# Kernel optimization log

Hardware: AMD Instinct MI355X
Metric: run time of the kernel (lower is better)

The kernel has to match this reference:

```python
import jax, jax.numpy as jnp
import numpy as np

NEG = -1000000.0  # mask fill value used by original sequence_mask

def setup_inputs() -> dict:
    key = jax.random.key(0)
    k1, k2, k3, k4 = jax.random.split(key, 4)
    B, S, D = 32, 2048, 64
    queries = jax.random.normal(k1, (B, S, D), dtype=jnp.float32)
    keys = jax.random.normal(k2, (B, S, D), dtype=jnp.float32)
    values = jax.random.normal(k3, (B, S, D), dtype=jnp.float32)
    valid_lens = jax.random.randint(k4, (B,), 1, S + 1, dtype=jnp.int64)
    return {"queries": queries, "keys": keys, "values": values, "valid_lens": valid_lens}

def reference(queries, keys, values, valid_lens):
    d = queries.shape[-1]
    # [B, Sq, Sk]
    scores = jnp.einsum('bqd,bkd->bqk', queries, keys) / jnp.sqrt(jnp.asarray(d, queries.dtype))
    # valid_lens is 1D: one length per batch row, broadcast over all query rows
    kv_idx = jnp.arange(scores.shape[-1])  # [Sk]
    mask = kv_idx[None, None, :] < valid_lens[:, None, None]  # [B,1,Sk] broadcast
    scores = jnp.where(mask, scores, jnp.asarray(NEG, scores.dtype))
    weights = jax.nn.softmax(scores, axis=-1)
    # dropout p=0.0 -> identity
    return jnp.einsum('bqk,bkd->bqd', weights, values)
```

## Files before the change

### kernel.cpp

```cpp
#include <hip/hip_runtime.h>
#include <hip/hip_bf16.h>

typedef __attribute__((ext_vector_type(8))) short bf16x8;
typedef __attribute__((ext_vector_type(4))) float f32x4;
typedef __attribute__((ext_vector_type(16))) float f32x16;

#define BATCH 32
#define SEQ   2048
#define PSTR  20
#define KSTR  72
#define VSTR  36
#define LOG2E 1.44269504088896340736f
#define QSCALE (0.125f * LOG2E)
#define NEGL  (-1000000.0f * LOG2E)

__device__ __forceinline__ unsigned int pk2(float lo, float hi) {
    __hip_bfloat162 h2 = __float22bfloat162_rn(make_float2(lo, hi));
    return *reinterpret_cast<unsigned int*>(&h2);
}

__device__ __forceinline__ void dma16(const short* g, short* l) {
    __builtin_amdgcn_global_load_lds((const __attribute__((address_space(1))) void*)g,
                                     (__attribute__((address_space(3))) void*)l, 16, 0, 0);
}

__device__ __forceinline__ void plswap(unsigned int& a, unsigned int& b) {
    asm volatile("v_permlane32_swap_b32 %0, %1" : "+v"(a), "+v"(b));
}

__global__ void prep_vl(const int* __restrict__ VL, int* __restrict__ meta) {
    __shared__ int sv[BATCH];
    const int t = threadIdx.x;
    int odd = (t < 16) ? VL[2 * t + 1] : 0;
    const bool is64 = (__ballot(odd != 0) == 0ULL);
    if (t < BATCH) {
        int x = is64 ? VL[2 * t] : VL[t];
        x = x < 0 ? 0 : (x > SEQ ? SEQ : x);
        sv[t] = x;
    }
    __syncthreads();
    if (t < BATCH) {
        const int x = sv[t];
        int rank = 0;
        for (int j = 0; j < BATCH; ++j) {
            const int y = sv[j];
            rank += (y > x) || (y == x && j < t);
        }
        meta[rank] = x;
        meta[BATCH + rank] = t;
    }
}

__global__ __launch_bounds__(256) void prepkv(const float* __restrict__ Kp,
                                              const float* __restrict__ Vp,
                                              const int* __restrict__ VL,
                                              short* __restrict__ Kb,
                                              short* __restrict__ Vt,
                                              int* __restrict__ meta) {
    __shared__ unsigned int l[64 * VSTR];
    __shared__ int sv[BATCH];
    __shared__ int svl;
    const int tid = threadIdx.x;
    if (blockIdx.x == BATCH * 32) {
        if (tid < 64) {
            int odd = (tid < 16) ? VL[2 * tid + 1] : 0;
            const bool is64 = (__ballot(odd != 0) == 0ULL);
            if (tid < BATCH) {
                int x = is64 ? VL[2 * tid] : VL[tid];
                x = x < 0 ? 0 : (x > SEQ ? SEQ : x);
                sv[tid] = x;
            }
            asm volatile("s_waitcnt lgkmcnt(0)" ::: "memory");
            if (tid < BATCH) {
                const int x = sv[tid];
                int rank = 0;
                for (int j = 0; j < BATCH; ++j) {
                    const int y = sv[j];
                    rank += (y > x) || (y == x && j < tid);
                }
                meta[rank] = x;
                meta[BATCH + rank] = tid;
            }
        }
        return;
    }
    const int b = blockIdx.x >> 5, kt = blockIdx.x & 31, kb = kt * 64;
    if (tid < 64) {
        int odd = (tid < 16) ? VL[2 * tid + 1] : 0;
        const bool is64 = (__ballot(odd != 0) == 0ULL);
        if (tid == 0) {
            int x = is64 ? VL[2 * b] : VL[b];
            x = x < 0 ? 0 : (x > SEQ ? SEQ : x);
            svl = x;
        }
    }
    __syncthreads();
    if (kb >= svl) return;
    const float* Kv = Kp + ((size_t)b * SEQ + kb) * 64;
    const float* Vb = Vp + ((size_t)b * SEQ + kb) * 64;
    #pragma unroll
    for (int h = 0; h < 4; ++h) {
        const int c = tid + h * 256;
        const int row = c >> 4, col = (c & 15) * 4;
        f32x4 x = *(const f32x4*)(Kv + row * 64 + col);
        unsigned int* dst = (unsigned int*)(Kb + ((size_t)b * SEQ + kb + row) * 64 + col);
        dst[0] = pk2(x[0], x[1]); dst[1] = pk2(x[2], x[3]);
    }
    #pragma unroll
    for (int h = 0; h < 2; ++h) {
        const int u = tid + h * 256;
        const int d4 = (u & 3) + ((u >> 7) << 2);
        const int kp = (u >> 2) & 31;
        f32x4 a = *(const f32x4*)(Vb + (2 * kp) * 64 + d4 * 4);
        f32x4 c = *(const f32x4*)(Vb + (2 * kp + 1) * 64 + d4 * 4);
        #pragma unroll
        for (int j = 0; j < 4; ++j)
            l[(d4 * 4 + j) * VSTR + kp] = pk2(a[j], c[j]);
    }
    __syncthreads();
    const int d = tid >> 2, cg = tid & 3;
    unsigned int w[8];
    #pragma unroll
    for (int j = 0; j < 8; ++j) w[j] = l[d * VSTR + cg * 8 + j];
    unsigned int* dst = (unsigned int*)Vt + ((size_t)(b * 32 + kt) * 64 + d) * 32 + cg * 8;
    #pragma unroll
    for (int j = 0; j < 8; ++j) dst[j] = w[j];
}

__global__ __launch_bounds__(256, 4)
void attn_fwd(const float* __restrict__ Qp, const short* __restrict__ Kb,
              const short* __restrict__ Vt, const int* __restrict__ meta,
              float* __restrict__ Out) {
    constexpr int S = SEQ;
    __shared__ short bK2[2 * 4096];
    __shared__ short bV3[3 * 4096];

    const int tid  = threadIdx.x;
    const int wave = tid >> 6, lane = tid & 63;
    const int r31 = lane & 31, hi = lane >> 5;
    const int l7  = lane & 7;
    const int qh = wave >> 1, kh = wave & 1;

    const int g  = blockIdx.x >> 8;
    const int k8 = (blockIdx.x >> 5) & 7;
    const int qt = blockIdx.x & 31;
    const int slot = (g << 3) + ((g & 1) ? 7 - k8 : k8);

    const int vl = meta[slot], batch = meta[BATCH + slot];
    const int ntiles = (vl + 63) >> 6;

    const short* Kbb = Kb + (size_t)batch * S * 64;
    const short* Vtb = Vt + (size_t)batch * 32 * 4096;

    const int r8 = lane >> 3, s8 = lane & 7, csw = s8 ^ r8;
    const short* gK0 = Kbb + (wave * 16 + r8) * 64 + csw * 8;
    const short* gV0 = Vtb + (wave * 16 + r8) * 64 + csw * 8;
    short* lK0 = &bK2[wave * 16 * 64];
    short* lV0 = &bV3[wave * 16 * 64];

    bf16x8 qf[4];
    {
        const float* qb = Qp + ((size_t)batch * S + qt * 64 + qh * 32 + r31) * 64 + hi * 8;
        #pragma unroll
        for (int kf = 0; kf < 4; ++kf) {
            f32x4 a = *(const f32x4*)(qb + kf * 16);
            f32x4 c = *(const f32x4*)(qb + kf * 16 + 4);
            union { bf16x8 v; unsigned int u[4]; } qq;
            qq.u[0] = pk2(a[0] * QSCALE, a[1] * QSCALE);
            qq.u[1] = pk2(a[2] * QSCALE, a[3] * QSCALE);
            qq.u[2] = pk2(c[0] * QSCALE, c[1] * QSCALE);
            qq.u[3] = pk2(c[2] * QSCALE, c[3] * QSCALE);
            qf[kf] = qq.v;
        }
    }

    f32x16 o0, o1, zv;
    #pragma unroll
    for (int r = 0; r < 16; ++r) { o0[r] = 0.f; o1[r] = 0.f; zv[r] = 0.f; }
    float lpart = 0.f;
    const int krow = kh * 32 + r31;

    int vP = 16384, vC = 0, vN = 8192;
    union { bf16x8 v; unsigned int u[4]; } pf0, pf1;

    if (ntiles > 0) {
        dma16(gK0,       lK0);
        dma16(gK0 + 512, lK0 + 512);
        dma16(gV0,       lV0);
        dma16(gV0 + 512, lV0 + 512);
    }

    for (int kt = 0; kt < ntiles; ++kt) {
        __syncthreads();
        if (kt + 1 < ntiles) {
            const int ko = (kt + 1) * 4096;
            short* ktgt = lK0 + (((kt + 1) & 1) << 12);
            short* vtgt = (short*)((char*)lV0 + vN);
            dma16(gK0 + ko,       ktgt);
            dma16(gK0 + ko + 512, ktgt + 512);
            dma16(gV0 + ko,       vtgt);
            dma16(gV0 + ko + 512, vtgt + 512);
        }

        const char* cK = (const char*)bK2 + ((kt & 1) << 13);
        f32x16 st;
        __builtin_amdgcn_s_setprio(1);
        {
            bf16x8 k0 = *(const bf16x8*)(cK + krow * 128 + (((0 + hi) ^ l7) << 4));
            bf16x8 k1 = *(const bf16x8*)(cK + krow * 128 + (((2 + hi) ^ l7) << 4));
            bf16x8 k2 = *(const bf16x8*)(cK + krow * 128 + (((4 + hi) ^ l7) << 4));
            bf16x8 k3 = *(const bf16x8*)(cK + krow * 128 + (((6 + hi) ^ l7) << 4));
            st = __builtin_amdgcn_mfma_f32_32x32x16_bf16(k0, qf[0], zv, 0, 0, 0);
            st = __builtin_amdgcn_mfma_f32_32x32x16_bf16(k1, qf[1], st, 0, 0, 0);
            st = __builtin_amdgcn_mfma_f32_32x32x16_bf16(k2, qf[2], st, 0, 0, 0);
            st = __builtin_amdgcn_mfma_f32_32x32x16_bf16(k3, qf[3], st, 0, 0, 0);
        }
        if (kt > 0) {
            const char* cV = (const char*)bV3 + vP;
            bf16x8 vf0 = *(const bf16x8*)(cV + r31 * 128 + (((kh * 4 + hi) ^ l7) << 4));
            o0 = __builtin_amdgcn_mfma_f32_32x32x16_bf16(vf0, pf0.v, o0, 0, 0, 0);
            bf16x8 vf1 = *(const bf16x8*)(cV + r31 * 128 + (((kh * 4 + 2 + hi) ^ l7) << 4));
            o0 = __builtin_amdgcn_mfma_f32_32x32x16_bf16(vf1, pf1.v, o0, 0, 0, 0);
            bf16x8 vf2 = *(const bf16x8*)(cV + (32 + r31) * 128 + (((kh * 4 + hi) ^ l7) << 4));
            o1 = __builtin_amdgcn_mfma_f32_32x32x16_bf16(vf2, pf0.v, o1, 0, 0, 0);
            bf16x8 vf3 = *(const bf16x8*)(cV + (32 + r31) * 128 + (((kh * 4 + 2 + hi) ^ l7) << 4));
            o1 = __builtin_amdgcn_mfma_f32_32x32x16_bf16(vf3, pf1.v, o1, 0, 0, 0);
        }
        __builtin_amdgcn_s_setprio(0);

        const int rem = vl - (kt * 64 + kh * 32);
        if (rem < 32) {
            #pragma unroll
            for (int r = 0; r < 16; ++r) {
                const int kl = 4 * hi + (r & 3) + 8 * (r >> 2);
                st[r] = (kl < rem) ? st[r] : NEGL;
            }
        }

        #pragma unroll
        for (int r = 0; r < 16; ++r) st[r] = exp2f(st[r]);
        {
            const float a0 = (st[0] + st[1]) + (st[2] + st[3]);
            const float a1 = (st[4] + st[5]) + (st[6] + st[7]);
            const float a2 = (st[8] + st[9]) + (st[10] + st[11]);
            const float a3 = (st[12] + st[13]) + (st[14] + st[15]);
            lpart += (a0 + a1) + (a2 + a3);
        }

        {
            unsigned int x0 = pk2(st[0], st[1]),   y0 = pk2(st[4], st[5]);
            unsigned int x1 = pk2(st[2], st[3]),   y1 = pk2(st[6], st[7]);
            plswap(x0, y0); plswap(x1, y1);
            pf0.u[0] = x0; pf0.u[1] = x1; pf0.u[2] = y0; pf0.u[3] = y1;
            unsigned int x2 = pk2(st[8], st[9]),   y2 = pk2(st[12], st[13]);
            unsigned int x3 = pk2(st[10], st[11]), y3 = pk2(st[14], st[15]);
            plswap(x2, y2); plswap(x3, y3);
            pf1.u[0] = x2; pf1.u[1] = x3; pf1.u[2] = y2; pf1.u[3] = y3;
        }

        const int t_ = vP; vP = vC; vC = vN; vN = t_;
    }

    {
        const char* cV = (const char*)bV3 + vP;
        __builtin_amdgcn_s_setprio(1);
        bf16x8 vf0 = *(const bf16x8*)(cV + r31 * 128 + (((kh * 4 + hi) ^ l7) << 4));
        o0 = __builtin_amdgcn_mfma_f32_32x32x16_bf16(vf0, pf0.v, o0, 0, 0, 0);
        bf16x8 vf1 = *(const bf16x8*)(cV + r31 * 128 + (((kh * 4 + 2 + hi) ^ l7) << 4));
        o0 = __builtin_amdgcn_mfma_f32_32x32x16_bf16(vf1, pf1.v, o0, 0, 0, 0);
        bf16x8 vf2 = *(const bf16x8*)(cV + (32 + r31) * 128 + (((kh * 4 + hi) ^ l7) << 4));
        o1 = __builtin_amdgcn_mfma_f32_32x32x16_bf16(vf2, pf0.v, o1, 0, 0, 0);
        bf16x8 vf3 = *(const bf16x8*)(cV + (32 + r31) * 128 + (((kh * 4 + 2 + hi) ^ l7) << 4));
        o1 = __builtin_amdgcn_mfma_f32_32x32x16_bf16(vf3, pf1.v, o1, 0, 0, 0);
        __builtin_amdgcn_s_setprio(0);
    }

    float lw = lpart + __shfl_xor(lpart, 32);

    __syncthreads();
    float* mrg = (float*)bK2;
    float* lm  = (float*)bV3;
    if (kh == 1) {
        #pragma unroll
        for (int r = 0; r < 16; ++r) mrg[qh * 2048 + r * 64 + lane] = o0[r];
        #pragma unroll
        for (int r = 0; r < 16; ++r) mrg[qh * 2048 + (16 + r) * 64 + lane] = o1[r];
        lm[qh * 64 + lane] = lw;
    }
    __syncthreads();
    if (kh == 0) {
        #pragma unroll
        for (int r = 0; r < 16; ++r) o0[r] += mrg[qh * 2048 + r * 64 + lane];
        #pragma unroll
        for (int r = 0; r < 16; ++r) o1[r] += mrg[qh * 2048 + (16 + r) * 64 + lane];
        lw += lm[qh * 64 + lane];
        const float inv = (lw > 0.f) ? 1.0f / lw : 0.f;
        const size_t orow = ((size_t)batch * S + qt * 64 + qh * 32 + r31) * 64;
        #pragma unroll
        for (int g4 = 0; g4 < 4; ++g4) {
            f32x4 w;
            #pragma unroll
            for (int j = 0; j < 4; ++j) w[j] = o0[g4 * 4 + j] * inv;
            *(f32x4*)(Out + orow + g4 * 8 + hi * 4) = w;
        }
        #pragma unroll
        for (int g4 = 0; g4 < 4; ++g4) {
            f32x4 w;
            #pragma unroll
            for (int j = 0; j < 4; ++j) w[j] = o1[g4 * 4 + j] * inv;
            *(f32x4*)(Out + orow + 32 + g4 * 8 + hi * 4) = w;
        }
    }
}

__device__ __forceinline__ void load_tile_fb(const float* __restrict__ Kb,
                                             const float* __restrict__ Vb,
                                             int tid, f32x4 kv[4], f32x4 vv[4]) {
    #pragma unroll
    for (int h = 0; h < 4; ++h) {
        const int c = tid + h * 256;
        kv[h] = *(const f32x4*)(Kb + (c >> 4) * 64 + (c & 15) * 4);
    }
    #pragma unroll
    for (int h = 0; h < 2; ++h) {
        const int u  = tid + h * 256;
        const int d4 = (u & 3) + ((u >> 7) << 2);
        const int kp = (u >> 2) & 31;
        vv[2 * h]     = *(const f32x4*)(Vb + (2 * kp) * 64 + d4 * 4);
        vv[2 * h + 1] = *(const f32x4*)(Vb + (2 * kp + 1) * 64 + d4 * 4);
    }
}

__global__ __launch_bounds__(256, 4)
void attn_fb(const float* __restrict__ Qp, const float* __restrict__ Kp,
             const float* __restrict__ Vp, const int* __restrict__ meta,
             float* __restrict__ Out) {
    constexpr int S = SEQ;
    constexpr int qtiles = S >> 6;
    __shared__ short        lK [64 * KSTR];
    __shared__ unsigned int lVt[64 * VSTR];
    __shared__ unsigned int lPt[4 * 32 * PSTR];
    const int tid = threadIdx.x;
    const int wave = tid >> 6, lane = tid & 63;
    const int l15 = lane & 15, grp = lane >> 4;
    const int slot = blockIdx.x / qtiles, qt = blockIdx.x % qtiles;
    const int vl = meta[slot], batch = meta[BATCH + slot];
    const int ntiles = (vl + 63) >> 6;
    const float* Kb = Kp + (size_t)batch * S * 64;
    const float* Vb = Vp + (size_t)batch * S * 64;
    bf16x8 qf[2];
    {
        const float* qb = Qp + ((size_t)batch * S + qt * 64 + wave * 16 + l15) * 64 + grp * 8;
        #pragma unroll
        for (int kf = 0; kf < 2; ++kf) {
            f32x4 a = *(const f32x4*)(qb + kf * 32);
            f32x4 b = *(const f32x4*)(qb + kf * 32 + 4);
            union { bf16x8 v; unsigned int u[4]; } qq;
            qq.u[0] = pk2(a[0], a[1]); qq.u[1] = pk2(a[2], a[3]);
            qq.u[2] = pk2(b[0], b[1]); qq.u[3] = pk2(b[2], b[3]);
            qf[kf] = qq.v;
        }
    }
    f32x4 o[4] = {{0.f,0.f,0.f,0.f},{0.f,0.f,0.f,0.f},{0.f,0.f,0.f,0.f},{0.f,0.f,0.f,0.f}};
    float mrun = -INFINITY, lrun = 0.f;
    unsigned int* pw = &lPt[wave * 32 * PSTR];
    f32x4 kv[4], vv[4];
    if (ntiles > 0) load_tile_fb(Kb, Vb, tid, kv, vv);
    for (int kt = 0; kt < ntiles; ++kt) {
        const int kb = kt * 64;
        __syncthreads();
        #pragma unroll
        for (int h = 0; h < 4; ++h) {
            const int c = tid + h * 256;
            const int row = c >> 4, col = (c & 15) * 4;
            union { f32x4 f; float e[4]; } x; x.f = kv[h];
            unsigned int* dst = (unsigned int*)&lK[row * KSTR + col];
            dst[0] = pk2(x.e[0], x.e[1]); dst[1] = pk2(x.e[2], x.e[3]);
        }
        #pragma unroll
        for (int h = 0; h < 2; ++h) {
            const int u  = tid + h * 256;
            const int d4 = (u & 3) + ((u >> 7) << 2);
            const int kp = (u >> 2) & 31;
            union { f32x4 f; float e[4]; } a, b;
            a.f = vv[2 * h]; b.f = vv[2 * h + 1];
            #pragma unroll
            for (int j = 0; j < 4; ++j)
                lVt[(d4 * 4 + j) * VSTR + kp] = pk2(a.e[j], b.e[j]);
        }
        if (kt + 1 < ntiles) load_tile_fb(Kb + (size_t)(kb + 64) * 64, Vb + (size_t)(kb + 64) * 64, tid, kv, vv);
        __syncthreads();
        f32x4 st[4] = {{0.f,0.f,0.f,0.f},{0.f,0.f,0.f,0.f},{0.f,0.f,0.f,0.f},{0.f,0.f,0.f,0.f}};
        #pragma unroll
        for (int kf = 0; kf < 2; ++kf) {
            #pragma unroll
            for (int ct = 0; ct < 4; ++ct) {
                bf16x8 kfr = *(const bf16x8*)&lK[(ct * 16 + l15) * KSTR + kf * 32 + grp * 8];
                st[ct] = __builtin_amdgcn_mfma_f32_16x16x32_bf16(kfr, qf[kf], st[ct], 0, 0, 0);
            }
        }
        #pragma unroll
        for (int ct = 0; ct < 4; ++ct)
            #pragma unroll
            for (int r = 0; r < 4; ++r) {
                const bool valid = (kb + ct * 16 + grp * 4 + r) < vl;
                st[ct][r] = valid ? st[ct][r] * (0.125f * LOG2E) : NEGL;
            }
        float t0 = fmaxf(fmaxf(st[0][0], st[0][1]), fmaxf(st[0][2], st[0][3]));
        float t1 = fmaxf(fmaxf(st[1][0], st[1][1]), fmaxf(st[1][2], st[1][3]));
        float t2 = fmaxf(fmaxf(st[2][0], st[2][1]), fmaxf(st[2][2], st[2][3]));
        float t3 = fmaxf(fmaxf(st[3][0], st[3][1]), fmaxf(st[3][2], st[3][3]));
        float tm = fmaxf(fmaxf(t0, t1), fmaxf(t2, t3));
        tm = fmaxf(tm, __shfl_xor(tm, 16));
        tm = fmaxf(tm, __shfl_xor(tm, 32));
        const float mnew  = fmaxf(mrun, tm);
        const float alpha = exp2f(mrun - mnew);
        mrun = mnew;
        lrun *= alpha;
        #pragma unroll
        for (int dt = 0; dt < 4; ++dt)
            #pragma unroll
            for (int r = 0; r < 4; ++r) o[dt][r] *= alpha;
        float rs = 0.f;
        #pragma unroll
        for (int ct = 0; ct < 4; ++ct) {
            #pragma unroll
            for (int r = 0; r < 4; ++r) {
                st[ct][r] = exp2f(st[ct][r] - mrun);
                rs += st[ct][r];
            }
            #pragma unroll
            for (int a = 0; a < 2; ++a)
                pw[(ct * 8 + grp * 2 + a) * PSTR + l15] = pk2(st[ct][2 * a], st[ct][2 * a + 1]);
        }
        rs += __shfl_xor(rs, 16);
        rs += __shfl_xor(rs, 32);
        lrun += rs;
        asm volatile("s_waitcnt lgkmcnt(0)" ::: "memory");
        #pragma unroll
        for (int kk = 0; kk < 2; ++kk) {
            union { bf16x8 v; unsigned int u[4]; } pf;
            #pragma unroll
            for (int jj = 0; jj < 4; ++jj)
                pf.u[jj] = pw[(kk * 16 + grp * 4 + jj) * PSTR + l15];
            #pragma unroll
            for (int dt = 0; dt < 4; ++dt) {
                bf16x8 vf = *(const bf16x8*)&lVt[(dt * 16 + l15) * VSTR + kk * 16 + grp * 4];
                o[dt] = __builtin_amdgcn_mfma_f32_16x16x32_bf16(vf, pf.v, o[dt], 0, 0, 0);
            }
        }
    }
    const float inv = (lrun > 0.f) ? 1.0f / lrun : 0.f;
    const size_t orow = ((size_t)batch * S + qt * 64 + wave * 16 + l15) * 64;
    #pragma unroll
    for (int dt = 0; dt < 4; ++dt) {
        f32x4 w = o[dt];
        w[0] *= inv; w[1] *= inv; w[2] *= inv; w[3] *= inv;
        *(f32x4*)(Out + orow + dt * 16 + grp * 4) = w;
    }
}

extern "C" void kernel_launch(void* const* d_in, const int* in_sizes, int n_in,
                              void* d_out, int out_size, void* d_ws, size_t ws_size,
                              hipStream_t stream) {
    const float* Q  = (const float*)d_in[0];
    const float* K  = (const float*)d_in[1];
    const float* V  = (const float*)d_in[2];
    const int*   VL = (const int*)d_in[3];
    int* meta = (int*)d_ws;
    const size_t need = 512 + 2 * (size_t)BATCH * SEQ * 64 * sizeof(short);
    dim3 block(256);
    if (ws_size >= need) {
        short* Kb = (short*)((char*)d_ws + 512);
        short* Vt = Kb + (size_t)BATCH * SEQ * 64;
        prepkv<<<dim3(BATCH * 32 + 1), block, 0, stream>>>(K, V, VL, Kb, Vt, meta);
        attn_fwd<<<dim3(BATCH * 32), block, 0, stream>>>(Q, Kb, Vt, meta, (float*)d_out);
    } else {
        prep_vl<<<1, 64, 0, stream>>>(VL, meta);
        attn_fb<<<dim3(BATCH * (SEQ >> 6)), block, 0, stream>>>(Q, K, V, meta, (float*)d_out);
    }
}
```

Baseline: 125.9 us.

## Widen attention blocks to 8 waves splitting 128-key chunks four ways

```diff
diff --git a/kernel.cpp b/kernel.cpp
--- a/kernel.cpp
+++ b/kernel.cpp
@@ -95,7 +95,7 @@
         }
     }
     __syncthreads();
-    if (kb >= svl) return;
+    if (kb >= ((svl + 127) & ~127)) return;
     const float* Kv = Kp + ((size_t)b * SEQ + kb) * 64;
     const float* Vb = Vp + ((size_t)b * SEQ + kb) * 64;
     #pragma unroll
@@ -127,27 +127,25 @@
     for (int j = 0; j < 8; ++j) dst[j] = w[j];
 }
 
-__global__ __launch_bounds__(256, 4)
+__global__ __launch_bounds__(512, 4)
 void attn_fwd(const float* __restrict__ Qp, const short* __restrict__ Kb,
               const short* __restrict__ Vt, const int* __restrict__ meta,
               float* __restrict__ Out) {
     constexpr int S = SEQ;
-    __shared__ short bK2[2 * 4096];
-    __shared__ short bV3[3 * 4096];
+    __shared__ short bK2[2 * 8192];
+    __shared__ short bV2[2 * 8192];
 
     const int tid  = threadIdx.x;
     const int wave = tid >> 6, lane = tid & 63;
     const int r31 = lane & 31, hi = lane >> 5;
     const int l7  = lane & 7;
-    const int qh = wave >> 1, kh = wave & 1;
-
-    const int g  = blockIdx.x >> 8;
-    const int k8 = (blockIdx.x >> 5) & 7;
-    const int qt = blockIdx.x & 31;
-    const int slot = (g << 3) + ((g & 1) ? 7 - k8 : k8);
+    const int qh = wave >> 2, kh = wave & 3;
+
+    const int slot = blockIdx.x >> 5;
+    const int qt   = blockIdx.x & 31;
 
     const int vl = meta[slot], batch = meta[BATCH + slot];
-    const int ntiles = (vl + 63) >> 6;
+    const int nchunks = (vl + 127) >> 7;
 
     const short* Kbb = Kb + (size_t)batch * S * 64;
     const short* Vtb = Vt + (size_t)batch * 32 * 4096;
@@ -156,7 +154,7 @@
     const short* gK0 = Kbb + (wave * 16 + r8) * 64 + csw * 8;
     const short* gV0 = Vtb + (wave * 16 + r8) * 64 + csw * 8;
     short* lK0 = &bK2[wave * 16 * 64];
-    short* lV0 = &bV3[wave * 16 * 64];
+    short* lV0 = &bV2[wave * 16 * 64];
 
     bf16x8 qf[4];
     {
@@ -179,121 +177,132 @@
     for (int r = 0; r < 16; ++r) { o0[r] = 0.f; o1[r] = 0.f; zv[r] = 0.f; }
     float lpart = 0.f;
     const int krow = kh * 32 + r31;
-
-    int vP = 16384, vC = 0, vN = 8192;
-    union { bf16x8 v; unsigned int u[4]; } pf0, pf1;
-
-    if (ntiles > 0) {
+    const int vrow0 = (kh >> 1) * 64 + r31;
+    const int vc0 = (kh & 1) * 4 + hi;
+
+    if (nchunks > 0) {
         dma16(gK0,       lK0);
         dma16(gK0 + 512, lK0 + 512);
         dma16(gV0,       lV0);
         dma16(gV0 + 512, lV0 + 512);
     }
 
-    for (int kt = 0; kt < ntiles; ++kt) {
+    for (int kt = 0; kt < nchunks; ++kt) {
         __syncthreads();
-        if (kt + 1 < ntiles) {
-            const int ko = (kt + 1) * 4096;
-            short* ktgt = lK0 + (((kt + 1) & 1) << 12);
-            short* vtgt = (short*)((char*)lV0 + vN);
+        if (kt + 1 < nchunks) {
+            const int ko = (kt + 1) * 8192;
+            short* ktgt = lK0 + (((kt + 1) & 1) << 13);
+            short* vtgt = lV0 + (((kt + 1) & 1) << 13);
             dma16(gK0 + ko,       ktgt);
             dma16(gK0 + ko + 512, ktgt + 512);
             dma16(gV0 + ko,       vtgt);
             dma16(gV0 + ko + 512, vtgt + 512);
         }
 
-        const char* cK = (const char*)bK2 + ((kt & 1) << 13);
-        f32x16 st;
-        __builtin_amdgcn_s_setprio(1);
-        {
-            bf16x8 k0 = *(const bf16x8*)(cK + krow * 128 + (((0 + hi) ^ l7) << 4));
-            bf16x8 k1 = *(const bf16x8*)(cK + krow * 128 + (((2 + hi) ^ l7) << 4));
-            bf16x8 k2 = *(const bf16x8*)(cK + krow * 128 + (((4 + hi) ^ l7) << 4));
-            bf16x8 k3 = *(const bf16x8*)(cK + krow * 128 + (((6 + hi) ^ l7) << 4));
-            st = __builtin_amdgcn_mfma_f32_32x32x16_bf16(k0, qf[0], zv, 0, 0, 0);
-            st = __builtin_amdgcn_mfma_f32_32x32x16_bf16(k1, qf[1], st, 0, 0, 0);
-            st = __builtin_amdgcn_mfma_f32_32x32x16_bf16(k2, qf[2], st, 0, 0, 0);
-            st = __builtin_amdgcn_mfma_f32_32x32x16_bf16(k3, qf[3], st, 0, 0, 0);
-        }
-        if (kt > 0) {
-            const char* cV = (const char*)bV3 + vP;
-            bf16x8 vf0 = *(const bf16x8*)(cV + r31 * 128 + (((kh * 4 + hi) ^ l7) << 4));
-            o0 = __builtin_amdgcn_mfma_f32_32x32x16_bf16(vf0, pf0.v, o0, 0, 0, 0);
-            bf16x8 vf1 = *(const bf16x8*)(cV + r31 * 128 + (((kh * 4 + 2 + hi) ^ l7) << 4));
-            o0 = __builtin_amdgcn_mfma_f32_32x32x16_bf16(vf1, pf1.v, o0, 0, 0, 0);
-            bf16x8 vf2 = *(const bf16x8*)(cV + (32 + r31) * 128 + (((kh * 4 + hi) ^ l7) << 4));
-            o1 = __builtin_amdgcn_mfma_f32_32x32x16_bf16(vf2, pf0.v, o1, 0, 0, 0);
-            bf16x8 vf3 = *(const bf16x8*)(cV + (32 + r31) * 128 + (((kh * 4 + 2 + hi) ^ l7) << 4));
-            o1 = __builtin_amdgcn_mfma_f32_32x32x16_bf16(vf3, pf1.v, o1, 0, 0, 0);
-        }
-        __builtin_amdgcn_s_setprio(0);
-
-        const int rem = vl - (kt * 64 + kh * 32);
-        if (rem < 32) {
-            #pragma unroll
-            for (int r = 0; r < 16; ++r) {
-                const int kl = 4 * hi + (r & 3) + 8 * (r >> 2);
-                st[r] = (kl < rem) ? st[r] : NEGL;
-            }
-        }
-
-        #pragma unroll
-        for (int r = 0; r < 16; ++r) st[r] = exp2f(st[r]);
-        {
-            const float a0 = (st[0] + st[1]) + (st[2] + st[3]);
-            const float a1 = (st[4] + st[5]) + (st[6] + st[7]);
-            const float a2 = (st[8] + st[9]) + (st[10] + st[11]);
-            const float a3 = (st[12] + st[13]) + (st[14] + st[15]);
-            lpart += (a0 + a1) + (a2 + a3);
-        }
-
-        {
-            unsigned int x0 = pk2(st[0], st[1]),   y0 = pk2(st[4], st[5]);
-            unsigned int x1 = pk2(st[2], st[3]),   y1 = pk2(st[6], st[7]);
-            plswap(x0, y0); plswap(x1, y1);
-            pf0.u[0] = x0; pf0.u[1] = x1; pf0.u[2] = y0; pf0.u[3] = y1;
-            unsigned int x2 = pk2(st[8], st[9]),   y2 = pk2(st[12], st[13]);
-            unsigned int x3 = pk2(st[10], st[11]), y3 = pk2(st[14], st[15]);
-            plswap(x2, y2); plswap(x3, y3);
-            pf1.u[0] = x2; pf1.u[1] = x3; pf1.u[2] = y2; pf1.u[3] = y3;
-        }
-
-        const int t_ = vP; vP = vC; vC = vN; vN = t_;
-    }
-
-    {
-        const char* cV = (const char*)bV3 + vP;
-        __builtin_amdgcn_s_setprio(1);
-        bf16x8 vf0 = *(const bf16x8*)(cV + r31 * 128 + (((kh * 4 + hi) ^ l7) << 4));
-        o0 = __builtin_amdgcn_mfma_f32_32x32x16_bf16(vf0, pf0.v, o0, 0, 0, 0);
-        bf16x8 vf1 = *(const bf16x8*)(cV + r31 * 128 + (((kh * 4 + 2 + hi) ^ l7) << 4));
-        o0 = __builtin_amdgcn_mfma_f32_32x32x16_bf16(vf1, pf1.v, o0, 0, 0, 0);
-        bf16x8 vf2 = *(const bf16x8*)(cV + (32 + r31) * 128 + (((kh * 4 + hi) ^ l7) << 4));
-        o1 = __builtin_amdgcn_mfma_f32_32x32x16_bf16(vf2, pf0.v, o1, 0, 0, 0);
-        bf16x8 vf3 = *(const bf16x8*)(cV + (32 + r31) * 128 + (((kh * 4 + 2 + hi) ^ l7) << 4));
-        o1 = __builtin_amdgcn_mfma_f32_32x32x16_bf16(vf3, pf1.v, o1, 0, 0, 0);
-        __builtin_amdgcn_s_setprio(0);
+        if (kt * 128 + kh * 32 < vl) {
+            const char* cK = (const char*)bK2 + ((kt & 1) << 14);
+            const char* cV = (const char*)bV2 + ((kt & 1) << 14);
+            f32x16 st;
+            __builtin_amdgcn_s_setprio(1);
+            {
+                bf16x8 k0 = *(const bf16x8*)(cK + krow * 128 + (((0 + hi) ^ l7) << 4));
+                bf16x8 k1 = *(const bf16x8*)(cK + krow * 128 + (((2 + hi) ^ l7) << 4));
+                bf16x8 k2 = *(const bf16x8*)(cK + krow * 128 + (((4 + hi) ^ l7) << 4));
+                bf16x8 k3 = *(const bf16x8*)(cK + krow * 128 + (((6 + hi) ^ l7) << 4));
+                st = __builtin_amdgcn_mfma_f32_32x32x16_bf16(k0, qf[0], zv, 0, 0, 0);
+                st = __builtin_amdgcn_mfma_f32_32x32x16_bf16(k1, qf[1], st, 0, 0, 0);
+                st = __builtin_amdgcn_mfma_f32_32x32x16_bf16(k2, qf[2], st, 0, 0, 0);
+                st = __builtin_amdgcn_mfma_f32_32x32x16_bf16(k3, qf[3], st, 0, 0, 0);
+            }
+            __builtin_amdgcn_s_setprio(0);
+
+            const int rem = vl - (kt * 128 + kh * 32);
+            if (rem < 32) {
+                #pragma unroll
+                for (int r = 0; r < 16; ++r) {
+                    const int kl = 4 * hi + (r & 3) + 8 * (r >> 2);
+                    st[r] = (kl < rem) ? st[r] : NEGL;
+                }
+            }
+
+            #pragma unroll
+            for (int r = 0; r < 16; ++r) st[r] = exp2f(st[r]);
+            {
+                const float a0 = (st[0] + st[1]) + (st[2] + st[3]);
+                const float a1 = (st[4] + st[5]) + (st[6] + st[7]);
+                const float a2 = (st[8] + st[9]) + (st[10] + st[11]);
+                const float a3 = (st[12] + st[13]) + (st[14] + st[15]);
+                lpart += (a0 + a1) + (a2 + a3);
+            }
+
+            union { bf16x8 v; unsigned int u[4]; } pf0, pf1;
+            {
+                unsigned int x0 = pk2(st[0], st[1]),   y0 = pk2(st[4], st[5]);
+                unsigned int x1 = pk2(st[2], st[3]),   y1 = pk2(st[6], st[7]);
+                plswap(x0, y0); plswap(x1, y1);
+                pf0.u[0] = x0; pf0.u[1] = x1; pf0.u[2] = y0; pf0.u[3] = y1;
+                unsigned int x2 = pk2(st[8], st[9]),   y2 = pk2(st[12], st[13]);
+                unsigned int x3 = pk2(st[10], st[11]), y3 = pk2(st[14], st[15]);
+                plswap(x2, y2); plswap(x3, y3);
+                pf1.u[0] = x2; pf1.u[1] = x3; pf1.u[2] = y2; pf1.u[3] = y3;
+            }
+
+            __builtin_amdgcn_s_setprio(1);
+            {
+                bf16x8 vf0 = *(const bf16x8*)(cV + vrow0 * 128 + ((vc0 ^ l7) << 4));
+                o0 = __builtin_amdgcn_mfma_f32_32x32x16_bf16(vf0, pf0.v, o0, 0, 0, 0);
+                bf16x8 vf1 = *(const bf16x8*)(cV + vrow0 * 128 + (((vc0 + 2) ^ l7) << 4));
+                o0 = __builtin_amdgcn_mfma_f32_32x32x16_bf16(vf1, pf1.v, o0, 0, 0, 0);
+                bf16x8 vf2 = *(const bf16x8*)(cV + (vrow0 + 32) * 128 + ((vc0 ^ l7) << 4));
+                o1 = __builtin_amdgcn_mfma_f32_32x32x16_bf16(vf2, pf0.v, o1, 0, 0, 0);
+                bf16x8 vf3 = *(const bf16x8*)(cV + (vrow0 + 32) * 128 + (((vc0 + 2) ^ l7) << 4));
+                o1 = __builtin_amdgcn_mfma_f32_32x32x16_bf16(vf3, pf1.v, o1, 0, 0, 0);
+            }
+            __builtin_amdgcn_s_setprio(0);
+        }
     }
 
     float lw = lpart + __shfl_xor(lpart, 32);
 
     __syncthreads();
-    float* mrg = (float*)bK2;
-    float* lm  = (float*)bV3;
-    if (kh == 1) {
-        #pragma unroll
-        for (int r = 0; r < 16; ++r) mrg[qh * 2048 + r * 64 + lane] = o0[r];
-        #pragma unroll
-        for (int r = 0; r < 16; ++r) mrg[qh * 2048 + (16 + r) * 64 + lane] = o1[r];
-        lm[qh * 64 + lane] = lw;
+    float* mA = (float*)bK2;
+    float* mB = (float*)bV2;
+    float* lA = (float*)bK2 + 4096;
+    float* lB = (float*)bV2 + 4096;
+    if (kh == 1 || kh == 3) {
+        float* m = (kh == 1) ? mA : mB;
+        float* lv = (kh == 1) ? lA : lB;
+        #pragma unroll
+        for (int r = 0; r < 16; ++r) m[qh * 2048 + r * 64 + lane] = o0[r];
+        #pragma unroll
+        for (int r = 0; r < 16; ++r) m[qh * 2048 + (16 + r) * 64 + lane] = o1[r];
+        lv[qh * 64 + lane] = lw;
+    }
+    __syncthreads();
+    if (kh == 0 || kh == 2) {
+        const float* m = (kh == 0) ? mA : mB;
+        const float* lv = (kh == 0) ? lA : lB;
+        #pragma unroll
+        for (int r = 0; r < 16; ++r) o0[r] += m[qh * 2048 + r * 64 + lane];
+        #pragma unroll
+        for (int r = 0; r < 16; ++r) o1[r] += m[qh * 2048 + (16 + r) * 64 + lane];
+        lw += lv[qh * 64 + lane];
+    }
+    __syncthreads();
+    if (kh == 2) {
+        #pragma unroll
+        for (int r = 0; r < 16; ++r) mA[qh * 2048 + r * 64 + lane] = o0[r];
+        #pragma unroll
+        for (int r = 0; r < 16; ++r) mA[qh * 2048 + (16 + r) * 64 + lane] = o1[r];
+        lA[qh * 64 + lane] = lw;
     }
     __syncthreads();
     if (kh == 0) {
         #pragma unroll
-        for (int r = 0; r < 16; ++r) o0[r] += mrg[qh * 2048 + r * 64 + lane];
-        #pragma unroll
-        for (int r = 0; r < 16; ++r) o1[r] += mrg[qh * 2048 + (16 + r) * 64 + lane];
-        lw += lm[qh * 64 + lane];
+        for (int r = 0; r < 16; ++r) o0[r] += mA[qh * 2048 + r * 64 + lane];
+        #pragma unroll
+        for (int r = 0; r < 16; ++r) o1[r] += mA[qh * 2048 + (16 + r) * 64 + lane];
+        lw += lA[qh * 64 + lane];
         const float inv = (lw > 0.f) ? 1.0f / lw : 0.f;
         const size_t orow = ((size_t)batch * S + qt * 64 + qh * 32 + r31) * 64;
         #pragma unroll
@@ -469,14 +478,13 @@
     const int*   VL = (const int*)d_in[3];
     int* meta = (int*)d_ws;
     const size_t need = 512 + 2 * (size_t)BATCH * SEQ * 64 * sizeof(short);
-    dim3 block(256);
     if (ws_size >= need) {
         short* Kb = (short*)((char*)d_ws + 512);
         short* Vt = Kb + (size_t)BATCH * SEQ * 64;
-        prepkv<<<dim3(BATCH * 32 + 1), block, 0, stream>>>(K, V, VL, Kb, Vt, meta);
-        attn_fwd<<<dim3(BATCH * 32), block, 0, stream>>>(Q, Kb, Vt, meta, (float*)d_out);
+        prepkv<<<dim3(BATCH * 32 + 1), dim3(256), 0, stream>>>(K, V, VL, Kb, Vt, meta);
+        attn_fwd<<<dim3(BATCH * 32), dim3(512), 0, stream>>>(Q, Kb, Vt, meta, (float*)d_out);
     } else {
         prep_vl<<<1, 64, 0, stream>>>(VL, meta);
-        attn_fb<<<dim3(BATCH * (SEQ >> 6)), block, 0, stream>>>(Q, K, V, meta, (float*)d_out);
-    }
-}
+        attn_fb<<<dim3(BATCH * (SEQ >> 6)), dim3(256), 0, stream>>>(Q, K, V, meta, (float*)d_out);
+    }
+}
```

After: 132.7 us. +5.4%, slower.
